# Optimization experiments

Measured on AMD Instinct MI355X. Metric: run time of the kernel, lower is better.

## Reference

```python
import jax, jax.numpy as jnp
import numpy as np

N, C = 8192, 4096
EPS = 1e-12


def setup_inputs() -> dict:
    key = jax.random.key(0)
    kx, ky = jax.random.split(key)
    act_X = jax.random.normal(kx, (N, C), dtype=jnp.float32)
    act_Y = jax.random.normal(ky, (N, C), dtype=jnp.float32)
    return {"act_X": act_X, "act_Y": act_Y}


def reference(act_X, act_Y):
    # softmax over class dim (dim=1 in the torch module)
    probs_X = jax.nn.softmax(act_X, axis=1)  # [N, C]
    probs_Y = jax.nn.softmax(act_Y, axis=1)  # [N, C]

    # approximate_entropy_cu: mean per-sample Shannon entropy (nats)
    entropy = jnp.mean(-jnp.sum(probs_X * jnp.log(probs_X + EPS), axis=1))

    # approximate_mi_cu: plug-in MI from batch-averaged joint distribution
    n = probs_X.shape[0]
    joint = jnp.einsum('nc,nd->cd', probs_X, probs_Y) / n  # [C, C]
    marg_X = jnp.mean(probs_X, axis=0)  # [C]
    marg_Y = jnp.mean(probs_Y, axis=0)  # [C]
    log_ratio = jnp.log(joint + EPS) - (jnp.log(marg_X + EPS)[:, None]
                                        + jnp.log(marg_Y + EPS)[None, :])
    mi = jnp.sum(joint * log_ratio)

    return jnp.stack([entropy, mi])  # shape [2]
```

## Files before the change

kernel.cpp:

```cpp
#include <hip/hip_runtime.h>
#include <hip/hip_bf16.h>
#include <stdint.h>

#define NROWS 8192
#define CDIM  4096
#define KDIM  8192
#define EPS   1e-12f

typedef __attribute__((ext_vector_type(8)))  int   v8i;
typedef __attribute__((ext_vector_type(4)))  int   v4i;
typedef __attribute__((ext_vector_type(4)))  float f32x4;
typedef __attribute__((ext_vector_type(2)))  float f32x2;

__device__ inline float wave_sum(float v) {
#pragma unroll
    for (int o = 32; o > 0; o >>= 1) v += __shfl_xor(v, o, 64);
    return v;
}
__device__ inline float wave_max(float v) {
#pragma unroll
    for (int o = 32; o > 0; o >>= 1) v = fmaxf(v, __shfl_xor(v, o, 64));
    return v;
}

__global__ __launch_bounds__(256) void row_quant_kernel(const float* __restrict__ X,
                                                        const float* __restrict__ Y,
                                                        unsigned char* __restrict__ QX,
                                                        unsigned char* __restrict__ QY,
                                                        float* __restrict__ entPart) {
    const int t = threadIdx.x, lane = t & 63, wave = t >> 6;
    const int row = blockIdx.x * 4 + wave;
    const bool isY = blockIdx.y != 0;
    const float4* s4 = (const float4*)((isY ? Y : X) + (size_t)row * CDIM);
    unsigned int* dst = (unsigned int*)((isY ? QY : QX) + (size_t)row * CDIM);
    float4 v[16];
#pragma unroll
    for (int i = 0; i < 16; i++) v[i] = s4[i * 64 + lane];
    float m = -3.0e38f;
#pragma unroll
    for (int i = 0; i < 16; i++)
        m = fmaxf(m, fmaxf(fmaxf(v[i].x, v[i].y), fmaxf(v[i].z, v[i].w)));
    m = wave_max(m);
    float Z = 0.f, S = 0.f;
#pragma unroll
    for (int i = 0; i < 16; i++) {
        float e;
        e = __expf(v[i].x - m); Z += e; S += e * v[i].x; v[i].x = e;
        e = __expf(v[i].y - m); Z += e; S += e * v[i].y; v[i].y = e;
        e = __expf(v[i].z - m); Z += e; S += e * v[i].z; v[i].z = e;
        e = __expf(v[i].w - m); Z += e; S += e * v[i].w; v[i].w = e;
    }
    Z = wave_sum(Z); S = wave_sum(S);
    __shared__ float sent[4];
    if (lane == 0) sent[wave] = m + __logf(Z) - S / Z;
    const float sc = 512.0f / Z;
#pragma unroll
    for (int i = 0; i < 16; i++) {
        unsigned int w0 = (unsigned int)__builtin_amdgcn_cvt_pk_fp8_f32(
            v[i].x * sc, v[i].y * sc, 0, false);
        w0 = (unsigned int)__builtin_amdgcn_cvt_pk_fp8_f32(
            v[i].z * sc, v[i].w * sc, (int)w0, true);
        dst[i * 64 + lane] = w0;
    }
    __syncthreads();
    if (t == 0 && !isY)
        entPart[blockIdx.x] = sent[0] + sent[1] + sent[2] + sent[3];
}

__global__ __launch_bounds__(256) void transpose_marg_kernel(
        const unsigned char* __restrict__ QX, const unsigned char* __restrict__ QY,
        unsigned char* __restrict__ QXT, unsigned char* __restrict__ QYT,
        float* __restrict__ margX, float* __restrict__ margY) {
    const bool isY = blockIdx.z != 0;
    const unsigned char* __restrict__ Q = isY ? QY : QX;
    unsigned char* __restrict__ QT = isY ? QYT : QXT;
    float* __restrict__ marg = isY ? margY : margX;

    __shared__ __align__(16) unsigned char tile[128 * 128];
    __shared__ float smarg[128];
    const int t = threadIdx.x;
    const int c0 = blockIdx.x * 128, n0 = blockIdx.y * 128;
    if (t < 128) smarg[t] = 0.f;
    __syncthreads();
    const int cq = (t & 31) * 4;
    const int nq = (t >> 5) * 16;
    const unsigned char* src = Q + (size_t)(n0 + nq) * CDIM + c0 + cq;
    unsigned int u[16];
#pragma unroll
    for (int i = 0; i < 16; i++)
        u[i] = *(const unsigned int*)(src + (size_t)i * CDIM);
#pragma unroll
    for (int j = 0; j < 4; j++) {
        const unsigned int sel = (unsigned)j | ((unsigned)(j + 4) << 8);
        unsigned int d0, d1, d2, d3;
        {
            unsigned int p01 = __builtin_amdgcn_perm(u[1], u[0], sel);
            unsigned int p23 = __builtin_amdgcn_perm(u[3], u[2], sel);
            d0 = __builtin_amdgcn_perm(p23, p01, 0x05040100u);
        }
        {
            unsigned int p01 = __builtin_amdgcn_perm(u[5], u[4], sel);
            unsigned int p23 = __builtin_amdgcn_perm(u[7], u[6], sel);
            d1 = __builtin_amdgcn_perm(p23, p01, 0x05040100u);
        }
        {
            unsigned int p01 = __builtin_amdgcn_perm(u[9], u[8], sel);
            unsigned int p23 = __builtin_amdgcn_perm(u[11], u[10], sel);
            d2 = __builtin_amdgcn_perm(p23, p01, 0x05040100u);
        }
        {
            unsigned int p01 = __builtin_amdgcn_perm(u[13], u[12], sel);
            unsigned int p23 = __builtin_amdgcn_perm(u[15], u[14], sel);
            d3 = __builtin_amdgcn_perm(p23, p01, 0x05040100u);
        }
        const int r = cq + j;
        uint4 o; o.x = d0; o.y = d1; o.z = d2; o.w = d3;
        *(uint4*)&tile[r * 128 + ((((nq >> 4) ^ ((r >> 2) & 7))) << 4)] = o;
        float s = 0.f;
        f32x2 a;
        a = __builtin_amdgcn_cvt_pk_f32_fp8((int)d0, false); s += a.x + a.y;
        a = __builtin_amdgcn_cvt_pk_f32_fp8((int)d0, true);  s += a.x + a.y;
        a = __builtin_amdgcn_cvt_pk_f32_fp8((int)d1, false); s += a.x + a.y;
        a = __builtin_amdgcn_cvt_pk_f32_fp8((int)d1, true);  s += a.x + a.y;
        a = __builtin_amdgcn_cvt_pk_f32_fp8((int)d2, false); s += a.x + a.y;
        a = __builtin_amdgcn_cvt_pk_f32_fp8((int)d2, true);  s += a.x + a.y;
        a = __builtin_amdgcn_cvt_pk_f32_fp8((int)d3, false); s += a.x + a.y;
        a = __builtin_amdgcn_cvt_pk_f32_fp8((int)d3, true);  s += a.x + a.y;
        atomicAdd(&smarg[r], s);
    }
    __syncthreads();
#pragma unroll
    for (int p = 0; p < 4; p++) {
        const int r = p * 32 + (t >> 3);
        const int k = t & 7;
        uint4 o = *(const uint4*)&tile[r * 128 + (((k ^ ((r >> 2) & 7))) << 4)];
        *(uint4*)(QT + (size_t)(c0 + r) * KDIM + n0 + k * 16) = o;
    }
    if (t < 128) atomicAdd(&marg[c0 + t], smarg[t]);
}

#define GLD16(g, l)                                                                   \
    __builtin_amdgcn_global_load_lds((const __attribute__((address_space(1))) unsigned int*)(g), \
                                     (__attribute__((address_space(3))) unsigned int*)(l), 16, 0, 0)

__global__ __launch_bounds__(256) void gemm_mi_kernel(const unsigned char* __restrict__ A,
                                                      const unsigned char* __restrict__ B,
                                                      float* __restrict__ S_out) {
    __shared__ __align__(16) unsigned char As[128 * 128];
    __shared__ __align__(16) unsigned char Bs[128 * 128];
    const int t = threadIdx.x;
    const int m0 = blockIdx.x * 128, n0 = blockIdx.y * 128;
    const int grow = (t >> 6) * 32 + ((t & 63) >> 3);
    const int gcol = (((t & 7) ^ ((t & 63) >> 3)) * 16);
    const unsigned char* ga = A + (size_t)(m0 + grow) * KDIM + gcol;
    const unsigned char* gb = B + (size_t)(n0 + grow) * KDIM + gcol;
    unsigned char* la = &As[(t >> 6) * 4096 + (t & 63) * 16];
    unsigned char* lb = &Bs[(t >> 6) * 4096 + (t & 63) * 16];
    const int lane = t & 63, wave = t >> 6;
    const int wm = (wave & 1) * 64, wn = (wave >> 1) * 64;
    const int fr = lane & 15, quad = lane >> 4;
    const int sw = fr & 7;
    const int off0 = ((2 * quad)     ^ sw) * 16;
    const int off1 = ((2 * quad + 1) ^ sw) * 16;
    const unsigned char* pA = &As[(wm + fr) * 128];
    const unsigned char* pB = &Bs[(wn + fr) * 128];
    f32x4 acc[4][4];
#pragma unroll
    for (int i = 0; i < 4; i++)
#pragma unroll
        for (int j = 0; j < 4; j++) { acc[i][j][0] = 0.f; acc[i][j][1] = 0.f; acc[i][j][2] = 0.f; acc[i][j][3] = 0.f; }

    for (int k0 = 0; k0 < KDIM; k0 += 128) {
#pragma unroll
        for (int i = 0; i < 4; i++) {
            GLD16(ga + (size_t)i * 8 * KDIM + k0, la + i * 1024);
            GLD16(gb + (size_t)i * 8 * KDIM + k0, lb + i * 1024);
        }
        __syncthreads();
        v8i af[4], bg[4];
#pragma unroll
        for (int i = 0; i < 4; i++) {
            v4i lo = *(const v4i*)(pA + i * 16 * 128 + off0);
            v4i hi = *(const v4i*)(pA + i * 16 * 128 + off1);
            af[i][0] = lo[0]; af[i][1] = lo[1]; af[i][2] = lo[2]; af[i][3] = lo[3];
            af[i][4] = hi[0]; af[i][5] = hi[1]; af[i][6] = hi[2]; af[i][7] = hi[3];
        }
#pragma unroll
        for (int j = 0; j < 4; j++) {
            v4i lo = *(const v4i*)(pB + j * 16 * 128 + off0);
            v4i hi = *(const v4i*)(pB + j * 16 * 128 + off1);
            bg[j][0] = lo[0]; bg[j][1] = lo[1]; bg[j][2] = lo[2]; bg[j][3] = lo[3];
            bg[j][4] = hi[0]; bg[j][5] = hi[1]; bg[j][6] = hi[2]; bg[j][7] = hi[3];
        }
#pragma unroll
        for (int i = 0; i < 4; i++)
#pragma unroll
            for (int j = 0; j < 4; j++)
                acc[i][j] = __builtin_amdgcn_mfma_scale_f32_16x16x128_f8f6f4(
                    af[i], bg[j], acc[i][j], 0 , 0 ,
                    0, 0x7f , 0, 0x7f );
        __syncthreads();
    }
    const float invS = 4.656612873077393e-10f;
    float loc = 0.f;
#pragma unroll
    for (int i = 0; i < 4; i++)
#pragma unroll
        for (int j = 0; j < 4; j++)
#pragma unroll
            for (int r = 0; r < 4; r++) {
                float v = acc[i][j][r] * invS;
                loc += v * __logf(v + EPS);
            }
    loc = wave_sum(loc);
    __shared__ float sred[4];
    if (lane == 0) sred[wave] = loc;
    __syncthreads();
    if (t == 0) atomicAdd(S_out, sred[0] + sred[1] + sred[2] + sred[3]);
}

__global__ __launch_bounds__(256) void finalize_kernel(const float* __restrict__ accums,
                                                       const float* __restrict__ entPart,
                                                       const float* __restrict__ margX,
                                                       const float* __restrict__ margY,
                                                       float* __restrict__ out) {
    const int t = threadIdx.x;
    const int lane = t & 63, w = t >> 6;
    const float invN = 1.0f / 8192.0f;
    const float invM = 1.0f / 4194304.0f;
    float sx = 0.f, sy = 0.f, se = 0.f;
    for (int c = t; c < CDIM; c += 256) {
        float mx = margX[c] * invM;
        float my = margY[c] * invM;
        sx += mx * __logf(mx + EPS);
        sy += my * __logf(my + EPS);
    }
    for (int c = t; c < 2048; c += 256) se += entPart[c];
    sx = wave_sum(sx); sy = wave_sum(sy); se = wave_sum(se);
    __shared__ float rx[4], ry[4], re[4];
    if (lane == 0) { rx[w] = sx; ry[w] = sy; re[w] = se; }
    __syncthreads();
    if (t == 0) {
        float SX = rx[0] + rx[1] + rx[2] + rx[3];
        float SY = ry[0] + ry[1] + ry[2] + ry[3];
        float SE = re[0] + re[1] + re[2] + re[3];
        out[0] = SE * invN;
        out[1] = accums[0] - SX - SY;
    }
}

extern "C" void kernel_launch(void* const* d_in, const int* in_sizes, int n_in,
                              void* d_out, int out_size, void* d_ws, size_t ws_size,
                              hipStream_t stream) {
    const float* X = (const float*)d_in[0];
    const float* Y = (const float*)d_in[1];
    char* ws = (char*)d_ws;
    unsigned char* QX  = (unsigned char*)ws;
    unsigned char* QY  = (unsigned char*)(ws + 33554432ll);
    unsigned char* QXT = (unsigned char*)(ws + 67108864ll);
    unsigned char* QYT = (unsigned char*)(ws + 100663296ll);
    float* margX = (float*)(ws + 134217728ll);
    float* margY = (float*)(ws + 134234112ll);
    float* accums = (float*)(ws + 134250496ll);
    float* entPart = (float*)(ws + 134250752ll);

    hipMemsetAsync(ws + 134217728ll, 0, 2 * 16384 + 256, stream);

    row_quant_kernel<<<dim3(2048, 2), 256, 0, stream>>>(X, Y, QX, QY, entPart);
    transpose_marg_kernel<<<dim3(CDIM / 128, NROWS / 128, 2), 256, 0, stream>>>(
        QX, QY, QXT, QYT, margX, margY);
    gemm_mi_kernel<<<dim3(CDIM / 128, CDIM / 128), 256, 0, stream>>>(QXT, QYT, &accums[0]);
    finalize_kernel<<<1, 256, 0, stream>>>(accums, entPart, margX, margY, (float*)d_out);
}
```

Measured before the change: 469.6 us.

## Double-buffer FP8 MI GEMM with 256x256 tiles and async LDS prefetch

Rewrites the FP8 MFMA GEMM so each 512-thread block computes a 256x256 output tile. It double-buffers 128-wide K slices in 128 KB of LDS, issuing global-to-LDS loads for the next slice while the current one is being multiplied. Waits use explicit vmcnt and raw barriers, and wave priority is raised around the MFMA section. The goal is to hide memory latency and halve operand reloads per output element. In exchange, the large LDS footprint limits the kernel to one block per CU and register pressure rises with the 8x4 accumulator array.

```diff
diff --git a/kernel.cpp b/kernel.cpp
--- a/kernel.cpp
+++ b/kernel.cpp
@@ -143,68 +143,94 @@
     __builtin_amdgcn_global_load_lds((const __attribute__((address_space(1))) unsigned int*)(g), \
                                      (__attribute__((address_space(3))) unsigned int*)(l), 16, 0, 0)
 
-__global__ __launch_bounds__(256) void gemm_mi_kernel(const unsigned char* __restrict__ A,
-                                                      const unsigned char* __restrict__ B,
-                                                      float* __restrict__ S_out) {
-    __shared__ __align__(16) unsigned char As[128 * 128];
-    __shared__ __align__(16) unsigned char Bs[128 * 128];
+#define BUFSZ 65536
+#define BOFS  32768
+
+__global__ __launch_bounds__(512, 2) void gemm_mi_kernel(const unsigned char* __restrict__ A,
+                                                         const unsigned char* __restrict__ B,
+                                                         float* __restrict__ S_out) {
+    __shared__ __align__(16) unsigned char lds[131072];
     const int t = threadIdx.x;
-    const int m0 = blockIdx.x * 128, n0 = blockIdx.y * 128;
-    const int grow = (t >> 6) * 32 + ((t & 63) >> 3);
-    const int gcol = (((t & 7) ^ ((t & 63) >> 3)) * 16);
-    const unsigned char* ga = A + (size_t)(m0 + grow) * KDIM + gcol;
-    const unsigned char* gb = B + (size_t)(n0 + grow) * KDIM + gcol;
-    unsigned char* la = &As[(t >> 6) * 4096 + (t & 63) * 16];
-    unsigned char* lb = &Bs[(t >> 6) * 4096 + (t & 63) * 16];
     const int lane = t & 63, wave = t >> 6;
-    const int wm = (wave & 1) * 64, wn = (wave >> 1) * 64;
-    const int fr = lane & 15, quad = lane >> 4;
-    const int sw = fr & 7;
+    const int m0 = blockIdx.x * 256, n0 = blockIdx.y * 256;
+
+    const int srow = wave * 32 + (lane >> 3);
+    const int gcol = ((lane & 7) ^ (lane >> 3)) * 16;
+    const unsigned char* ga = A + (size_t)(m0 + srow) * KDIM + gcol;
+    const unsigned char* gb = B + (size_t)(n0 + srow) * KDIM + gcol;
+    const int loff = wave * 4096 + lane * 16;
+
+    const int wm = (wave >> 2) * 128, wn = (wave & 3) * 64;
+    const int fr = lane & 15, quad = lane >> 4, sw = fr & 7;
     const int off0 = ((2 * quad)     ^ sw) * 16;
     const int off1 = ((2 * quad + 1) ^ sw) * 16;
-    const unsigned char* pA = &As[(wm + fr) * 128];
-    const unsigned char* pB = &Bs[(wn + fr) * 128];
-    f32x4 acc[4][4];
-#pragma unroll
-    for (int i = 0; i < 4; i++)
+
+    f32x4 acc[8][4];
+#pragma unroll
+    for (int i = 0; i < 8; i++)
 #pragma unroll
         for (int j = 0; j < 4; j++) { acc[i][j][0] = 0.f; acc[i][j][1] = 0.f; acc[i][j][2] = 0.f; acc[i][j][3] = 0.f; }
 
-    for (int k0 = 0; k0 < KDIM; k0 += 128) {
-#pragma unroll
-        for (int i = 0; i < 4; i++) {
-            GLD16(ga + (size_t)i * 8 * KDIM + k0, la + i * 1024);
-            GLD16(gb + (size_t)i * 8 * KDIM + k0, lb + i * 1024);
-        }
-        __syncthreads();
-        v8i af[4], bg[4];
-#pragma unroll
-        for (int i = 0; i < 4; i++) {
-            v4i lo = *(const v4i*)(pA + i * 16 * 128 + off0);
-            v4i hi = *(const v4i*)(pA + i * 16 * 128 + off1);
-            af[i][0] = lo[0]; af[i][1] = lo[1]; af[i][2] = lo[2]; af[i][3] = lo[3];
-            af[i][4] = hi[0]; af[i][5] = hi[1]; af[i][6] = hi[2]; af[i][7] = hi[3];
-        }
+#pragma unroll
+    for (int i = 0; i < 4; i++) {
+        GLD16(ga + (size_t)i * 8 * KDIM, lds + loff + i * 1024);
+        GLD16(gb + (size_t)i * 8 * KDIM, lds + BOFS + loff + i * 1024);
+    }
+
+    int cur = 0;
+    for (int tt = 0; tt < KDIM / 128; ++tt) {
+        if (tt + 1 < KDIM / 128) {
+            const int nb = (cur ^ 1) * BUFSZ;
+            const int kn = (tt + 1) * 128;
+#pragma unroll
+            for (int i = 0; i < 4; i++) {
+                GLD16(ga + (size_t)i * 8 * KDIM + kn, lds + nb + loff + i * 1024);
+                GLD16(gb + (size_t)i * 8 * KDIM + kn, lds + nb + BOFS + loff + i * 1024);
+            }
+            asm volatile("s_waitcnt vmcnt(8)" ::: "memory");
+        } else {
+            asm volatile("s_waitcnt vmcnt(0)" ::: "memory");
+        }
+        asm volatile("s_barrier" ::: "memory");
+        __builtin_amdgcn_sched_barrier(0);
+
+        const unsigned char* base = lds + cur * BUFSZ;
+        v8i bg[4];
 #pragma unroll
         for (int j = 0; j < 4; j++) {
-            v4i lo = *(const v4i*)(pB + j * 16 * 128 + off0);
-            v4i hi = *(const v4i*)(pB + j * 16 * 128 + off1);
+            const unsigned char* pB = base + BOFS + (wn + j * 16 + fr) * 128;
+            v4i lo = *(const v4i*)(pB + off0);
+            v4i hi = *(const v4i*)(pB + off1);
             bg[j][0] = lo[0]; bg[j][1] = lo[1]; bg[j][2] = lo[2]; bg[j][3] = lo[3];
             bg[j][4] = hi[0]; bg[j][5] = hi[1]; bg[j][6] = hi[2]; bg[j][7] = hi[3];
         }
-#pragma unroll
-        for (int i = 0; i < 4; i++)
+        __builtin_amdgcn_s_setprio(1);
+#pragma unroll
+        for (int i = 0; i < 8; i++) {
+            const unsigned char* pA = base + (wm + i * 16 + fr) * 128;
+            v4i lo = *(const v4i*)(pA + off0);
+            v4i hi = *(const v4i*)(pA + off1);
+            v8i af;
+            af[0] = lo[0]; af[1] = lo[1]; af[2] = lo[2]; af[3] = lo[3];
+            af[4] = hi[0]; af[5] = hi[1]; af[6] = hi[2]; af[7] = hi[3];
 #pragma unroll
             for (int j = 0; j < 4; j++)
                 acc[i][j] = __builtin_amdgcn_mfma_scale_f32_16x16x128_f8f6f4(
-                    af[i], bg[j], acc[i][j], 0 , 0 ,
+                    af, bg[j], acc[i][j], 0 , 0 ,
                     0, 0x7f , 0, 0x7f );
-        __syncthreads();
-    }
+        }
+        __builtin_amdgcn_s_setprio(0);
+        __builtin_amdgcn_sched_barrier(0);
+        asm volatile("s_waitcnt lgkmcnt(0)" ::: "memory");
+        asm volatile("s_barrier" ::: "memory");
+        __builtin_amdgcn_sched_barrier(0);
+        cur ^= 1;
+    }
+
     const float invS = 4.656612873077393e-10f;
     float loc = 0.f;
 #pragma unroll
-    for (int i = 0; i < 4; i++)
+    for (int i = 0; i < 8; i++)
 #pragma unroll
         for (int j = 0; j < 4; j++)
 #pragma unroll
@@ -213,10 +239,15 @@
                 loc += v * __logf(v + EPS);
             }
     loc = wave_sum(loc);
-    __shared__ float sred[4];
+    __shared__ float sred[8];
     if (lane == 0) sred[wave] = loc;
     __syncthreads();
-    if (t == 0) atomicAdd(S_out, sred[0] + sred[1] + sred[2] + sred[3]);
+    if (t == 0) {
+        float s = 0.f;
+#pragma unroll
+        for (int w = 0; w < 8; w++) s += sred[w];
+        atomicAdd(S_out, s);
+    }
 }
 
 __global__ __launch_bounds__(256) void finalize_kernel(const float* __restrict__ accums,
@@ -269,6 +300,6 @@
     row_quant_kernel<<<dim3(2048, 2), 256, 0, stream>>>(X, Y, QX, QY, entPart);
     transpose_marg_kernel<<<dim3(CDIM / 128, NROWS / 128, 2), 256, 0, stream>>>(
         QX, QY, QXT, QYT, margX, margY);
-    gemm_mi_kernel<<<dim3(CDIM / 128, CDIM / 128), 256, 0, stream>>>(QXT, QYT, &accums[0]);
+    gemm_mi_kernel<<<dim3(CDIM / 256, CDIM / 256), 512, 0, stream>>>(QXT, QYT, &accums[0]);
     finalize_kernel<<<1, 256, 0, stream>>>(accums, entPart, margX, margY, (float*)d_out);
 }
```

After: 457.3 us. -2.6%, faster.
